# Kernel tuning notes

Measured on AMD Instinct MI355X. Metric: run time of the kernel, lower is better.

## Reference

```python
import jax, jax.numpy as jnp
import numpy as np

B, S, D = 1, 4096, 512      # batch, seq, model dim
E, K, H = 64, 2, 256        # routed experts, top-k, expert hidden (moe_inter_dim)
HS = 2048                   # shared expert hidden = n_shared_experts * inter_dim
EPS = 1e-5                  # LayerNorm eps (torch default)


def setup_inputs() -> dict:
    key = jax.random.key(0)
    ks = jax.random.split(key, 16)
    n = lambda k, shp, s=0.02: jax.random.normal(k, shp, dtype=jnp.float32) * s
    return {
        "x": jax.random.normal(ks[0], (B, S, D), dtype=jnp.float32),
        # gate Linear(dim -> E)
        "Wg": n(ks[1], (E, D)), "bg": n(ks[2], (E,)),
        # per-expert LayerNorm affine
        "gamma": 1.0 + n(ks[3], (E, D)), "beta": n(ks[4], (E, D)),
        # per-expert SwiGLU: w1, w3: D->H ; w2: H->D
        "W1": n(ks[5], (E, D, H)), "b1": n(ks[6], (E, H)),
        "W3": n(ks[7], (E, D, H)), "b3": n(ks[8], (E, H)),
        "W2": n(ks[9], (E, H, D)), "b2": n(ks[10], (E, D)),
        # shared expert (same Expert structure, hidden HS)
        "gs": 1.0 + n(ks[11], (D,)), "bs": n(ks[11], (D,)),
        "Ws1": n(ks[12], (D, HS)), "bs1": n(ks[12], (HS,)),
        "Ws3": n(ks[13], (D, HS)), "bs3": n(ks[13], (HS,)),
        "Ws2": n(ks[14], (HS, D)), "bs2": n(ks[15], (D,)),
    }


def reference(x, Wg, bg, gamma, beta, W1, b1, W3, b3, W2, b2,
              gs, bs, Ws1, bs1, Ws3, bs3, Ws2, bs2):
    shape = x.shape
    xt = x.reshape(-1, D)                      # [T, D] tokens
    T = xt.shape[0]

    # ---- Gate (eval path: sigmoid scores, no load balancing / bias / groups) ----
    scores = jax.nn.sigmoid(xt @ Wg.T + bg)    # [T, E]
    w, idx = jax.lax.top_k(scores, K)          # [T, K]
    w = w / w.sum(-1, keepdims=True)           # sigmoid path normalization; route_scale = 1
    # dense combine weights: cw[t, e] = routing weight of token t on expert e (0 if not routed)
    cw = jnp.zeros((T, E), xt.dtype).at[jnp.arange(T)[:, None], idx].add(w)

    # ---- Shared LayerNorm statistics (affine folded per-expert below) ----
    mu = xt.mean(-1, keepdims=True)
    var = ((xt - mu) ** 2).mean(-1, keepdims=True)
    nx = (xt - mu) * jax.lax.rsqrt(var + EPS)  # [T, D], unit-affine normalized

    # Fold each expert's LN affine (gamma_e, beta_e) into its w1/w3:
    # (nx*g + b) @ W = nx @ (g[:,None]*W) + b @ W
    W1p = gamma[:, :, None] * W1
    b1p = b1 + jnp.einsum('ed,edh->eh', beta, W1)
    W3p = gamma[:, :, None] * W3
    b3p = b3 + jnp.einsum('ed,edh->eh', beta, W3)

    h1 = jnp.einsum('td,edh->eth', nx, W1p) + b1p[:, None, :]   # [E, T, H]
    h3 = jnp.einsum('td,edh->eth', nx, W3p) + b3p[:, None, :]
    h = jax.nn.silu(h1) * h3                                     # SwiGLU, [E, T, H]

    # Weighted combine: y[t] = sum_e cw[t,e] * (h[e,t] @ W2[e] + b2[e])
    hw = h * cw.T[:, :, None]                                    # [E, T, H]
    y = jnp.einsum('eth,ehd->td', hw, W2) + cw @ b2              # [T, D]

    # ---- Shared expert (applied to every token) ----
    nxs = nx * gs + bs
    hs = jax.nn.silu(nxs @ Ws1 + bs1) * (nxs @ Ws3 + bs3)        # [T, HS]
    z = hs @ Ws2 + bs2

    return (y + z).reshape(shape)
```

## Files before the change

### kernel.cpp

```cpp
#include <hip/hip_runtime.h>
#include <math.h>

typedef unsigned short u16;
typedef unsigned int u32;
typedef __attribute__((ext_vector_type(8))) short bf16x8;
typedef __attribute__((ext_vector_type(4))) float f32x4;

#define TT   4096
#define DM   512
#define NE   64
#define HE   256
#define HSH  2048
#define NSH  8
#define PADBASE 16384
#define MAXTILES 384

#define WAITV(N) asm volatile("s_waitcnt vmcnt(" #N ")" ::: "memory")
#define SBAR()   __builtin_amdgcn_s_barrier()
#define SCHEDB() __builtin_amdgcn_sched_barrier(0)

__device__ __forceinline__ float sig_(float z){ return 1.f/(1.f+__expf(-z)); }

__device__ __forceinline__ u16 f2bf(float x){
  u32 u = __builtin_bit_cast(u32, x);
  u = (u + 0x7FFFu + ((u >> 16) & 1u)) >> 16;
  return (u16)u;
}

__device__ __forceinline__ f32x4 mfma16(bf16x8 a, bf16x8 b, f32x4 c){
  return __builtin_amdgcn_mfma_f32_16x16x32_bf16(a, b, c, 0, 0, 0);
}

__device__ __forceinline__ bf16x8 frd(const char* tile, int row, int csw){
  return *(const bf16x8*)(tile + row*64 + csw);
}

__device__ __forceinline__ void gl16(const void* g, void* l){
  __builtin_amdgcn_global_load_lds(
      (const __attribute__((address_space(1))) unsigned int*)g,
      (__attribute__((address_space(3))) unsigned int*)l, 16, 0, 0);
}

template<int K, int N, bool FOLD>
__device__ __forceinline__ void cvt_tile(
    const float* __restrict__ in, const float* __restrict__ scale,
    const float* __restrict__ fvec, u16* __restrict__ out,
    float* __restrict__ fout, int local, int tid, char* LT)
{
  const int nbk = K >> 6;
  const int nbn = N >> 8;
  const int pm = nbk * nbn;
  const int z = local / pm, rem = local - z*pm;
  const int kt = rem % nbk, ntile = rem / nbk;
  const int k0 = kt*64;
  const int q = tid >> 6;
  const int t = tid & 63;
  const int nb = t*4;

  const float* src = in + (size_t)z*K*N + (size_t)(k0 + q*16)*N + ntile*256 + nb;
  const float* scp = scale ? (scale + (size_t)z*K + k0 + q*16) : nullptr;
  const float* fvp = fvec  ? (fvec  + (size_t)z*K + k0 + q*16) : nullptr;

  u32 pk[4][8];
  float fs0=0.f, fs1=0.f, fs2=0.f, fs3=0.f;
  #pragma unroll
  for (int j = 0; j < 16; j++){
    float4 v = *(const float4*)(src + (size_t)j*N);
    const float sc = scp ? scp[j] : 1.0f;
    const u32 b0 = f2bf(v.x*sc), b1 = f2bf(v.y*sc);
    const u32 b2 = f2bf(v.z*sc), b3 = f2bf(v.w*sc);
    if (j & 1){
      pk[0][j>>1] |= b0 << 16; pk[1][j>>1] |= b1 << 16;
      pk[2][j>>1] |= b2 << 16; pk[3][j>>1] |= b3 << 16;
    } else {
      pk[0][j>>1] = b0; pk[1][j>>1] = b1;
      pk[2][j>>1] = b2; pk[3][j>>1] = b3;
    }
    if (FOLD){
      const float fv = fvp[j];
      fs0 += v.x*fv; fs1 += v.y*fv; fs2 += v.z*fv; fs3 += v.w*fv;
    }
  }
  #pragma unroll
  for (int i = 0; i < 4; i++){
    const int n = nb + i;
    char* rowp = LT + n*144;
    const int x = (n >> 3) & 7;
    *(uint4*)(rowp + (((2*q)  ^x))*16) = *(const uint4*)&pk[i][0];
    *(uint4*)(rowp + (((2*q+1)^x))*16) = *(const uint4*)&pk[i][4];
  }
  if (FOLD){
    float* fb = fout + (size_t)z*N + ntile*256 + nb;
    atomicAdd(fb+0, fs0); atomicAdd(fb+1, fs1);
    atomicAdd(fb+2, fs2); atomicAdd(fb+3, fs3);
  }
  __syncthreads();

  u16* obase = out + (size_t)z*K*N + (size_t)(ntile*256)*K + k0;
  #pragma unroll 2
  for (int cc = 0; cc < 8; cc++){
    const int g = cc*256 + tid;
    const int row = g >> 3, ch = g & 7;
    uint4 v = *(const uint4*)(LT + row*144 + ((ch ^ ((row>>3)&7))*16));
    *(uint4*)(obase + (size_t)row*K + ch*8) = v;
  }
}

__global__ __launch_bounds__(256) void k_pre(
    const float* __restrict__ W1, const float* __restrict__ W3,
    const float* __restrict__ W2, const float* __restrict__ Ws1,
    const float* __restrict__ Ws3, const float* __restrict__ Ws2,
    const float* __restrict__ gamma, const float* __restrict__ beta,
    const float* __restrict__ gs, const float* __restrict__ bsv,
    u16* __restrict__ W1bT, u16* __restrict__ W3bT, u16* __restrict__ W2bT,
    u16* __restrict__ Ws1bT, u16* __restrict__ Ws3bT, u16* __restrict__ Ws2bT,
    float* __restrict__ b1f, float* __restrict__ b3f,
    const float* __restrict__ x, const float* __restrict__ Wg,
    const float* __restrict__ bg,
    u16* __restrict__ nxb, int* __restrict__ top_idx, float* __restrict__ top_w)
{
  __shared__ __align__(16) char LT[256*144];
  const int bid = blockIdx.x;
  const int tid = threadIdx.x;

  if (bid < 1728){
    if      (bid < 512)  cvt_tile<DM,HE, true >(W1,  gamma,   beta,    W1bT,  b1f,        bid,      tid, LT);
    else if (bid < 1024) cvt_tile<DM,HE, true >(W3,  gamma,   beta,    W3bT,  b3f,        bid-512,  tid, LT);
    else if (bid < 1536) cvt_tile<HE,DM, false>(W2,  nullptr, nullptr, W2bT,  nullptr,    bid-1024, tid, LT);
    else if (bid < 1600) cvt_tile<DM,HSH,true >(Ws1, gs,      bsv,     Ws1bT, b1f+NE*HE,  bid-1536, tid, LT);
    else if (bid < 1664) cvt_tile<DM,HSH,true >(Ws3, gs,      bsv,     Ws3bT, b3f+NE*HE,  bid-1600, tid, LT);
    else                 cvt_tile<HSH,DM,false>(Ws2, nullptr, nullptr, Ws2bT, nullptr,    bid-1664, tid, LT);
    return;
  }

  __shared__ float xs[DM];
  __shared__ float sred[4], ssred[4];
  __shared__ float sc[NE];
  const int t = bid - 1728;

  float2 v = reinterpret_cast<const float2*>(x + (size_t)t*DM)[tid];
  xs[2*tid]   = v.x;
  xs[2*tid+1] = v.y;
  float s  = v.x + v.y;
  float ss = v.x*v.x + v.y*v.y;
  #pragma unroll
  for (int o = 32; o > 0; o >>= 1){ s += __shfl_xor(s, o); ss += __shfl_xor(ss, o); }
  const int wid = tid >> 6, lane = tid & 63;
  if (lane == 0){ sred[wid] = s; ssred[wid] = ss; }
  __syncthreads();
  const float tot = sred[0]+sred[1]+sred[2]+sred[3];
  const float tss = ssred[0]+ssred[1]+ssred[2]+ssred[3];
  const float mu  = tot * (1.f/DM);
  const float var = tss * (1.f/DM) - mu*mu;
  const float rstd = rsqrtf(var + 1e-5f);
  u32 pk = (u32)f2bf((v.x-mu)*rstd) | ((u32)f2bf((v.y-mu)*rstd) << 16);
  *(u32*)(nxb + (size_t)t*DM + 2*tid) = pk;

  const int e = tid >> 2, sub = tid & 3;
  const float4* wrow4 = reinterpret_cast<const float4*>(Wg + (size_t)e*DM);
  const float4* xs4   = reinterpret_cast<const float4*>(xs);
  float acc = 0.f;
  #pragma unroll 4
  for (int i = sub; i < DM/4; i += 4){
    const float4 w = wrow4[i]; const float4 xv = xs4[i];
    acc += xv.x*w.x + xv.y*w.y + xv.z*w.z + xv.w*w.w;
  }
  acc += __shfl_xor(acc, 1);
  acc += __shfl_xor(acc, 2);
  if (sub == 0) sc[e] = acc + bg[e];
  __syncthreads();

  if (tid < 64) {
    const float s0 = sc[tid];
    float m = s0; int mi = tid;
    #pragma unroll
    for (int o = 1; o < 64; o <<= 1){
      float om = __shfl_xor(m, o); int oi = __shfl_xor(mi, o);
      if (om > m || (om == m && oi < mi)) { m = om; mi = oi; }
    }
    float s1 = (tid == mi) ? -INFINITY : s0;
    float m2 = s1; int mi2 = tid;
    #pragma unroll
    for (int o = 1; o < 64; o <<= 1){
      float om = __shfl_xor(m2, o); int oi = __shfl_xor(mi2, o);
      if (om > m2 || (om == m2 && oi < mi2)) { m2 = om; mi2 = oi; }
    }
    if (tid == 0){
      const float w0 = sig_(m), w1 = sig_(m2);
      const float inv = 1.f/(w0+w1);
      top_idx[2*t]   = mi;
      top_idx[2*t+1] = mi2;
      top_w[2*t]     = w0*inv;
      top_w[2*t+1]   = w1*inv;
    }
  }
}

__global__ __launch_bounds__(256) void k_route(
    const int* __restrict__ top_idx, const float* __restrict__ top_w,
    int* __restrict__ bucket_tok, float* __restrict__ bucket_w,
    int* __restrict__ tiles, int* __restrict__ n_tiles)
{
  __shared__ int cnt[NE], base_[NE];
  __shared__ int nroute;
  const int tid = threadIdx.x;
  if (tid < NE) cnt[tid] = 0;
  __syncthreads();
  for (int p = tid; p < TT*2; p += 256) atomicAdd(&cnt[top_idx[p]], 1);
  __syncthreads();
  if (tid == 0){
    int run = 0, ntl = 0;
    for (int e = 0; e < NE; e++){
      base_[e] = run;
      const int c = cnt[e];
      for (int b = 0; b < c; b += 128){
        const int n = (c - b < 128) ? (c - b) : 128;
        tiles[ntl++] = (e << 17) | (((run + b) >> 7) << 8) | n;
      }
      run += ((c + 127) >> 7) << 7;
    }
    nroute = ntl;
    n_tiles[0] = ntl + NSH*(TT/128);
    n_tiles[1] = ntl;
  }
  __syncthreads();
  if (tid < NSH*(TT/128)){
    const int s = tid >> 5, t = tid & 31;
    const int b0 = PADBASE + s*TT + t*128;
    tiles[nroute + tid] = ((NE + s) << 17) | ((b0 >> 7) << 8) | 128;
  }
  if (tid < NE) cnt[tid] = 0;
  __syncthreads();
  for (int p = tid; p < TT*2; p += 256){
    const int e = top_idx[p];
    const int pos = base_[e] + atomicAdd(&cnt[e], 1);
    bucket_tok[pos] = p >> 1;
    bucket_w[pos]   = top_w[p];
  }
}

__global__ __launch_bounds__(512) void k_up(
    const u16* __restrict__ nxb,
    const u16* __restrict__ W1bT, const u16* __restrict__ W3bT,
    const u16* __restrict__ Ws1bT, const u16* __restrict__ Ws3bT,
    const float* __restrict__ b1, const float* __restrict__ b3,
    const float* __restrict__ bs1, const float* __restrict__ bs3,
    const float* __restrict__ b1f, const float* __restrict__ b3f,
    const int* __restrict__ bucket_tok, const float* __restrict__ bucket_w,
    const int* __restrict__ tiles, const int* __restrict__ n_tiles,
    u16* __restrict__ hrout, u16* __restrict__ hs)
{
  if ((int)blockIdx.x >= n_tiles[0]) return;
  const int info = tiles[blockIdx.x];
  const int e  = info >> 17;
  const int b0 = ((info >> 8) & 0x1FF) << 7;
  const int nt = info & 255;
  const bool sh = (e >= NE);
  const int y  = blockIdx.y;

  __shared__ __align__(16) char Ab[2][8192];
  __shared__ __align__(16) char B1b[2][8192];
  __shared__ __align__(16) char B3b[2][8192];
  __shared__ int   toks[128];
  __shared__ float tw[128];

  const int tid = threadIdx.x, wid = tid >> 6, lane = tid & 63;
  const int l15 = lane & 15, q = lane >> 4;

  if (tid < 128){
    int tk; float w;
    if (!sh){
      if (tid < nt){ tk = bucket_tok[b0+tid]; w = bucket_w[b0+tid]; }
      else         { tk = 0; w = 0.f; }
    } else {
      tk = ((b0 - PADBASE) & (TT-1)) + tid; w = 1.f;
    }
    toks[tid] = tk; tw[tid] = w;
  }
  __syncthreads();

  const u16* w1e = sh ? (Ws1bT + (size_t)(e-NE)*HE*DM) : (W1bT + (size_t)e*HE*DM);
  const u16* w3e = sh ? (Ws3bT + (size_t)(e-NE)*HE*DM) : (W3bT + (size_t)e*HE*DM);

  const int srow = lane >> 2;
  const int csrc = (((lane & 3) ^ ((lane >> 3) & 3))) * 8;
  const u16* asrc = nxb + (size_t)toks[wid*16 + srow]*DM + csrc;
  const u16* b1s  = w1e + (size_t)(y*128 + wid*16 + srow)*DM + csrc;
  const u16* b3s  = w3e + (size_t)(y*128 + wid*16 + srow)*DM + csrc;
  const int loff = wid*1024;

#define UP_STAGE(ph, k0) do{ \
    gl16(asrc + (k0), Ab[ph] + loff); \
    gl16(b1s  + (k0), B1b[ph] + loff); \
    gl16(b3s  + (k0), B3b[ph] + loff); \
  } while(0)

  const int wm = (wid & 1)*64, wn = (wid >> 1)*32;

  const float* ob1 = sh ? (bs1 + (size_t)(e-NE)*HE) : (b1 + (size_t)e*HE);
  const float* ob3 = sh ? (bs3 + (size_t)(e-NE)*HE) : (b3 + (size_t)e*HE);
  f32x4 acc1[4][2], acc3[4][2];
  #pragma unroll
  for (int fn = 0; fn < 2; fn++){
    const int h = y*128 + wn + fn*16 + l15;
    const float v1 = ob1[h] + b1f[(size_t)e*HE + h];
    const float v3 = ob3[h] + b3f[(size_t)e*HE + h];
    #pragma unroll
    for (int fm = 0; fm < 4; fm++){
      acc1[fm][fn] = (f32x4){v1,v1,v1,v1};
      acc3[fm][fn] = (f32x4){v3,v3,v3,v3};
    }
  }

  UP_STAGE(0, 0);
  const int csw = (q ^ ((l15 >> 1) & 3)) * 16;

  for (int ks = 0; ks < DM/32; ks++){
    const int cur = ks & 1;
    WAITV(0);
    SBAR();
    if (ks + 1 < DM/32){ UP_STAGE(cur^1, (ks+1)*32); SCHEDB(); }
    const char* A  = Ab[cur];
    const char* B1 = B1b[cur];
    const char* B3 = B3b[cur];
    __builtin_amdgcn_s_setprio(1);
    bf16x8 fa[4];
    #pragma unroll
    for (int fm = 0; fm < 4; fm++) fa[fm] = frd(A, wm + fm*16 + l15, csw);
    #pragma unroll
    for (int fn = 0; fn < 2; fn++){
      bf16x8 fb1 = frd(B1, wn + fn*16 + l15, csw);
      bf16x8 fb3 = frd(B3, wn + fn*16 + l15, csw);
      #pragma unroll
      for (int fm = 0; fm < 4; fm++){
        acc1[fm][fn] = mfma16(fa[fm], fb1, acc1[fm][fn]);
        acc3[fm][fn] = mfma16(fa[fm], fb3, acc3[fm][fn]);
      }
    }
    __builtin_amdgcn_s_setprio(0);
  }
#undef UP_STAGE

  const int tbase = sh ? ((b0 - PADBASE) & (TT-1)) : 0;
  const int scol  = sh ? (e - NE)*HE : 0;
  #pragma unroll
  for (int fm = 0; fm < 4; fm++){
    #pragma unroll
    for (int fn = 0; fn < 2; fn++){
      const int hl = y*128 + wn + fn*16 + l15;
      #pragma unroll
      for (int r = 0; r < 4; r++){
        const int m = wm + fm*16 + 4*q + r;
        float v = 0.f;
        if (m < nt){
          const float a1 = acc1[fm][fn][r];
          const float a3 = acc3[fm][fn][r];
          v = a1 * sig_(a1) * a3 * tw[m];
        }
        if (sh) hs[(size_t)(tbase+m)*HSH + scol + hl] = f2bf(v);
        else    hrout[(size_t)(b0+m)*HE + hl] = f2bf(v);
      }
    }
  }
}

__global__ __launch_bounds__(512) void k_down(
    const u16* __restrict__ hs, const u16* __restrict__ Ws2bT,
    const float* __restrict__ bs2,
    const u16* __restrict__ hrout, const u16* __restrict__ W2bT,
    const float* __restrict__ b2,
    const int* __restrict__ bucket_tok, const float* __restrict__ bucket_w,
    const int* __restrict__ tiles, const int* __restrict__ n_tiles,
    float* __restrict__ out)
{
  __shared__ __align__(16) char Ab[2][8192];
  __shared__ __align__(16) char Bb[2][16384];
  __shared__ int   toks[128];
  __shared__ float tw[128];

  const int tid = threadIdx.x, wid = tid >> 6, lane = tid & 63;
  const int l15 = lane & 15, q = lane >> 4;
  const int csw  = (q ^ ((l15 >> 1) & 3)) * 16;
  const int srow = tid >> 2;
  const int csrc = ((tid & 3) ^ ((tid >> 3) & 3)) * 8;
  const int loff = wid*1024;
  const int wm = (wid & 1)*64, wn = (wid >> 1)*64;

  const u16* asrc; const u16* bsrc0; const u16* bsrc1;
  int nsteps, nt, d0;
  bool shpath;
  int e = 0, b0 = 0, kc = 0;

  if ((int)blockIdx.x < 256){
    shpath = true;
    kc = blockIdx.x & 3;
    d0 = ((blockIdx.x >> 2) & 1) * 256;
    const int t0 = (blockIdx.x >> 3) * 128;
    nsteps = 16; nt = 128;
    asrc  = hs    + (size_t)(t0 + srow)*HSH + kc*512 + csrc;
    bsrc0 = Ws2bT + (size_t)(d0 + srow)*HSH + kc*512 + csrc;
    bsrc1 = Ws2bT + (size_t)(d0 + 128 + srow)*HSH + kc*512 + csrc;
    if (tid < 128){ toks[tid] = t0 + tid; tw[tid] = 1.f; }
  } else {
    shpath = false;
    const int rb = (int)blockIdx.x - 256;
    const int ti = rb >> 1;
    if (ti >= n_tiles[1]) return;
    const int info = tiles[ti];
    e  = info >> 17;
    b0 = ((info >> 8) & 0x1FF) << 7;
    nt = info & 255;
    d0 = (rb & 1) * 256;
    nsteps = 8;
    const u16* w2e = W2bT + (size_t)e*DM*HE;
    asrc  = hrout + (size_t)(b0 + srow)*HE + csrc;
    bsrc0 = w2e + (size_t)(d0 + srow)*HE + csrc;
    bsrc1 = w2e + (size_t)(d0 + 128 + srow)*HE + csrc;
    if (tid < 128){
      if (tid < nt){ toks[tid] = bucket_tok[b0+tid]; tw[tid] = bucket_w[b0+tid]; }
      else         { toks[tid] = 0; tw[tid] = 0.f; }
    }
  }
  const size_t lda = shpath ? HSH : HE;
  (void)lda;
  __syncthreads();

#define DN_STAGE(ph, k0) do{ \
    gl16(asrc  + (k0), Ab[ph] + loff); \
    gl16(bsrc0 + (k0), Bb[ph] + loff); \
    gl16(bsrc1 + (k0), Bb[ph] + 8192 + loff); \
  } while(0)

  f32x4 acc[4][4];
  #pragma unroll
  for (int fm = 0; fm < 4; fm++)
    #pragma unroll
    for (int fn = 0; fn < 4; fn++) acc[fm][fn] = (f32x4){0.f,0.f,0.f,0.f};

  DN_STAGE(0, 0);

  for (int ks = 0; ks < nsteps; ks++){
    const int cur = ks & 1;
    WAITV(0);
    SBAR();
    if (ks + 1 < nsteps){ DN_STAGE(cur^1, (ks+1)*32); SCHEDB(); }
    const char* A = Ab[cur];
    const char* B = Bb[cur];
    __builtin_amdgcn_s_setprio(1);
    bf16x8 fa[4];
    #pragma unroll
    for (int fm = 0; fm < 4; fm++) fa[fm] = frd(A, wm + fm*16 + l15, csw);
    #pragma unroll
    for (int fn = 0; fn < 4; fn++){
      bf16x8 fb = frd(B, wn + fn*16 + l15, csw);
      #pragma unroll
      for (int fm = 0; fm < 4; fm++)
        acc[fm][fn] = mfma16(fa[fm], fb, acc[fm][fn]);
    }
    __builtin_amdgcn_s_setprio(0);
  }
#undef DN_STAGE

  #pragma unroll
  for (int fm = 0; fm < 4; fm++){
    #pragma unroll
    for (int fn = 0; fn < 4; fn++){
      const int d = d0 + wn + fn*16 + l15;
      float badd;
      if (shpath) badd = (kc == 0) ? bs2[d] : 0.f;
      else        badd = 0.f;
      #pragma unroll
      for (int r = 0; r < 4; r++){
        const int m = wm + fm*16 + 4*q + r;
        if (m < nt){
          const float extra = shpath ? badd : tw[m]*b2[(size_t)e*DM + d];
          atomicAdd(out + (size_t)toks[m]*DM + d, acc[fm][fn][r] + extra);
        }
      }
    }
  }
}

extern "C" void kernel_launch(void* const* d_in, const int* in_sizes, int n_in,
                              void* d_out, int out_size, void* d_ws, size_t ws_size,
                              hipStream_t stream)
{
  (void)in_sizes; (void)n_in; (void)ws_size;
  const float* x     = (const float*)d_in[0];
  const float* Wg    = (const float*)d_in[1];
  const float* bg    = (const float*)d_in[2];
  const float* gamma = (const float*)d_in[3];
  const float* beta  = (const float*)d_in[4];
  const float* W1    = (const float*)d_in[5];
  const float* b1    = (const float*)d_in[6];
  const float* W3    = (const float*)d_in[7];
  const float* b3    = (const float*)d_in[8];
  const float* W2    = (const float*)d_in[9];
  const float* b2    = (const float*)d_in[10];
  const float* gs    = (const float*)d_in[11];
  const float* bs    = (const float*)d_in[12];
  const float* Ws1   = (const float*)d_in[13];
  const float* bs1   = (const float*)d_in[14];
  const float* Ws3   = (const float*)d_in[15];
  const float* bs3   = (const float*)d_in[16];
  const float* Ws2   = (const float*)d_in[17];
  const float* bs2   = (const float*)d_in[18];
  float* out = (float*)d_out;

  char* ws = (char*)d_ws;
  size_t off = 0;
  auto alloc = [&](size_t bytes) -> char* {
    char* p = ws + off;
    off += (bytes + 255) & ~(size_t)255;
    return p;
  };
  u16*   nxb        = (u16*)  alloc((size_t)TT*DM*2);
  int*   top_idx    = (int*)  alloc((size_t)TT*2*4);
  float* top_w      = (float*)alloc((size_t)TT*2*4);
  int*   bucket_tok = (int*)  alloc((size_t)PADBASE*4);
  float* bucket_w   = (float*)alloc((size_t)PADBASE*4);
  int*   tiles      = (int*)  alloc(MAXTILES*4);
  int*   n_tiles    = (int*)  alloc(64);
  u16*   hrout      = (u16*)  alloc((size_t)PADBASE*HE*2);
  u16*   hs         = (u16*)  alloc((size_t)TT*HSH*2);
  u16*   W1bT       = (u16*)  alloc((size_t)NE*HE*DM*2);
  u16*   W3bT       = (u16*)  alloc((size_t)NE*HE*DM*2);
  u16*   W2bT       = (u16*)  alloc((size_t)NE*DM*HE*2);
  u16*   Ws1bT      = (u16*)  alloc((size_t)HSH*DM*2);
  u16*   Ws3bT      = (u16*)  alloc((size_t)HSH*DM*2);
  u16*   Ws2bT      = (u16*)  alloc((size_t)DM*HSH*2);
  float* b1f        = (float*)alloc((size_t)(NE*HE + HSH)*4);
  float* b3f        = (float*)alloc((size_t)(NE*HE + HSH)*4);

  hipMemsetAsync(b1f, 0, (size_t)(NE*HE + HSH)*4, stream);
  hipMemsetAsync(b3f, 0, (size_t)(NE*HE + HSH)*4, stream);
  hipMemsetAsync(out, 0, (size_t)out_size*sizeof(float), stream);

  k_pre<<<dim3(1728 + TT), 256, 0, stream>>>(
      W1, W3, W2, Ws1, Ws3, Ws2, gamma, beta, gs, bs,
      W1bT, W3bT, W2bT, Ws1bT, Ws3bT, Ws2bT, b1f, b3f,
      x, Wg, bg, nxb, top_idx, top_w);

  k_route<<<dim3(1), 256, 0, stream>>>(top_idx, top_w, bucket_tok, bucket_w, tiles, n_tiles);

  k_up<<<dim3(MAXTILES, 2), 512, 0, stream>>>(nxb, W1bT, W3bT, Ws1bT, Ws3bT,
                                              b1, b3, bs1, bs3, b1f, b3f,
                                              bucket_tok, bucket_w, tiles, n_tiles, hrout, hs);
  k_down<<<dim3(512), 512, 0, stream>>>(hs, Ws2bT, bs2, hrout, W2bT, b2,
                                        bucket_tok, bucket_w, tiles, n_tiles, out);
}
```

Measured before the change: 205.1 us.

## Shrink k_down tiles to 128x128 with 256 threads and batch cvt_tile loads

The down-projection kernel goes from 512-thread blocks computing 128x256 output tiles to 256-thread blocks computing 128x128 tiles, which doubles the grid and halves shared memory per block. The aim is more blocks in flight and better occupancy. The cost is that each A tile is loaded twice as often across the grid, and the number of atomic adds stays the same. Separately, the weight-conversion prologue now issues eight float4 loads at a time and loads the scale and fold vectors as float4, so more memory requests are in flight together.

Result: slower. 225.1 us (+9.8%).

```diff
diff --git a/kernel.cpp b/kernel.cpp
--- a/kernel.cpp
+++ b/kernel.cpp
@@ -58,29 +58,45 @@
   const int nb = t*4;
 
   const float* src = in + (size_t)z*K*N + (size_t)(k0 + q*16)*N + ntile*256 + nb;
-  const float* scp = scale ? (scale + (size_t)z*K + k0 + q*16) : nullptr;
-  const float* fvp = fvec  ? (fvec  + (size_t)z*K + k0 + q*16) : nullptr;
+  const float* scp = FOLD ? (scale + (size_t)z*K + k0 + q*16) : nullptr;
+  const float* fvp = FOLD ? (fvec  + (size_t)z*K + k0 + q*16) : nullptr;
 
   u32 pk[4][8];
   float fs0=0.f, fs1=0.f, fs2=0.f, fs3=0.f;
-  #pragma unroll
-  for (int j = 0; j < 16; j++){
-    float4 v = *(const float4*)(src + (size_t)j*N);
-    const float sc = scp ? scp[j] : 1.0f;
-    const u32 b0 = f2bf(v.x*sc), b1 = f2bf(v.y*sc);
-    const u32 b2 = f2bf(v.z*sc), b3 = f2bf(v.w*sc);
-    if (j & 1){
-      pk[0][j>>1] |= b0 << 16; pk[1][j>>1] |= b1 << 16;
-      pk[2][j>>1] |= b2 << 16; pk[3][j>>1] |= b3 << 16;
-    } else {
-      pk[0][j>>1] = b0; pk[1][j>>1] = b1;
-      pk[2][j>>1] = b2; pk[3][j>>1] = b3;
-    }
+
+  #pragma unroll
+  for (int half = 0; half < 2; half++){
+    float4 v[8];
+    #pragma unroll
+    for (int j = 0; j < 8; j++)
+      v[j] = *(const float4*)(src + (size_t)(half*8 + j)*N);
+    float scv[8], fvv[8];
     if (FOLD){
-      const float fv = fvp[j];
-      fs0 += v.x*fv; fs1 += v.y*fv; fs2 += v.z*fv; fs3 += v.w*fv;
-    }
-  }
+      *(float4*)&scv[0] = *(const float4*)(scp + half*8);
+      *(float4*)&scv[4] = *(const float4*)(scp + half*8 + 4);
+      *(float4*)&fvv[0] = *(const float4*)(fvp + half*8);
+      *(float4*)&fvv[4] = *(const float4*)(fvp + half*8 + 4);
+    }
+    #pragma unroll
+    for (int j = 0; j < 8; j++){
+      const int jj = half*8 + j;
+      const float sc = FOLD ? scv[j] : 1.0f;
+      const u32 b0 = f2bf(v[j].x*sc), b1 = f2bf(v[j].y*sc);
+      const u32 b2 = f2bf(v[j].z*sc), b3 = f2bf(v[j].w*sc);
+      if (jj & 1){
+        pk[0][jj>>1] |= b0 << 16; pk[1][jj>>1] |= b1 << 16;
+        pk[2][jj>>1] |= b2 << 16; pk[3][jj>>1] |= b3 << 16;
+      } else {
+        pk[0][jj>>1] = b0; pk[1][jj>>1] = b1;
+        pk[2][jj>>1] = b2; pk[3][jj>>1] = b3;
+      }
+      if (FOLD){
+        const float fv = fvv[j];
+        fs0 += v[j].x*fv; fs1 += v[j].y*fv; fs2 += v[j].z*fv; fs3 += v[j].w*fv;
+      }
+    }
+  }
+
   #pragma unroll
   for (int i = 0; i < 4; i++){
     const int n = nb + i;
@@ -364,7 +380,7 @@
   }
 }
 
-__global__ __launch_bounds__(512) void k_down(
+__global__ __launch_bounds__(256) void k_down(
     const u16* __restrict__ hs, const u16* __restrict__ Ws2bT,
     const float* __restrict__ bs2,
     const u16* __restrict__ hrout, const u16* __restrict__ W2bT,
@@ -374,7 +390,7 @@
     float* __restrict__ out)
 {
   __shared__ __align__(16) char Ab[2][8192];
-  __shared__ __align__(16) char Bb[2][16384];
+  __shared__ __align__(16) char Bb[2][8192];
   __shared__ int   toks[128];
   __shared__ float tw[128];
 
@@ -386,49 +402,50 @@
   const int loff = wid*1024;
   const int wm = (wid & 1)*64, wn = (wid >> 1)*64;
 
-  const u16* asrc; const u16* bsrc0; const u16* bsrc1;
+  const u16 *asrc, *asrc2, *bsrc, *bsrc2;
   int nsteps, nt, d0;
   bool shpath;
-  int e = 0, b0 = 0, kc = 0;
-
-  if ((int)blockIdx.x < 256){
+  int e = 0, kc = 0;
+
+  if ((int)blockIdx.x < 512){
     shpath = true;
     kc = blockIdx.x & 3;
-    d0 = ((blockIdx.x >> 2) & 1) * 256;
-    const int t0 = (blockIdx.x >> 3) * 128;
+    d0 = ((blockIdx.x >> 2) & 3) * 128;
+    const int t0 = (blockIdx.x >> 4) * 128;
     nsteps = 16; nt = 128;
     asrc  = hs    + (size_t)(t0 + srow)*HSH + kc*512 + csrc;
-    bsrc0 = Ws2bT + (size_t)(d0 + srow)*HSH + kc*512 + csrc;
-    bsrc1 = Ws2bT + (size_t)(d0 + 128 + srow)*HSH + kc*512 + csrc;
+    asrc2 = asrc  + (size_t)64*HSH;
+    bsrc  = Ws2bT + (size_t)(d0 + srow)*HSH + kc*512 + csrc;
+    bsrc2 = bsrc  + (size_t)64*HSH;
     if (tid < 128){ toks[tid] = t0 + tid; tw[tid] = 1.f; }
   } else {
     shpath = false;
-    const int rb = (int)blockIdx.x - 256;
-    const int ti = rb >> 1;
+    const int rb = (int)blockIdx.x - 512;
+    const int ti = rb >> 2;
     if (ti >= n_tiles[1]) return;
     const int info = tiles[ti];
     e  = info >> 17;
-    b0 = ((info >> 8) & 0x1FF) << 7;
+    const int b0 = ((info >> 8) & 0x1FF) << 7;
     nt = info & 255;
-    d0 = (rb & 1) * 256;
+    d0 = (rb & 3) * 128;
     nsteps = 8;
     const u16* w2e = W2bT + (size_t)e*DM*HE;
     asrc  = hrout + (size_t)(b0 + srow)*HE + csrc;
-    bsrc0 = w2e + (size_t)(d0 + srow)*HE + csrc;
-    bsrc1 = w2e + (size_t)(d0 + 128 + srow)*HE + csrc;
+    asrc2 = asrc  + (size_t)64*HE;
+    bsrc  = w2e + (size_t)(d0 + srow)*HE + csrc;
+    bsrc2 = bsrc + (size_t)64*HE;
     if (tid < 128){
       if (tid < nt){ toks[tid] = bucket_tok[b0+tid]; tw[tid] = bucket_w[b0+tid]; }
       else         { toks[tid] = 0; tw[tid] = 0.f; }
     }
   }
-  const size_t lda = shpath ? HSH : HE;
-  (void)lda;
   __syncthreads();
 
 #define DN_STAGE(ph, k0) do{ \
     gl16(asrc  + (k0), Ab[ph] + loff); \
-    gl16(bsrc0 + (k0), Bb[ph] + loff); \
-    gl16(bsrc1 + (k0), Bb[ph] + 8192 + loff); \
+    gl16(asrc2 + (k0), Ab[ph] + 4096 + loff); \
+    gl16(bsrc  + (k0), Bb[ph] + loff); \
+    gl16(bsrc2 + (k0), Bb[ph] + 4096 + loff); \
   } while(0)
 
   f32x4 acc[4][4];
@@ -466,9 +483,7 @@
     #pragma unroll
     for (int fn = 0; fn < 4; fn++){
       const int d = d0 + wn + fn*16 + l15;
-      float badd;
-      if (shpath) badd = (kc == 0) ? bs2[d] : 0.f;
-      else        badd = 0.f;
+      const float badd = shpath ? ((kc == 0) ? bs2[d] : 0.f) : 0.f;
       #pragma unroll
       for (int r = 0; r < 4; r++){
         const int m = wm + fm*16 + 4*q + r;
@@ -546,6 +561,6 @@
   k_up<<<dim3(MAXTILES, 2), 512, 0, stream>>>(nxb, W1bT, W3bT, Ws1bT, Ws3bT,
                                               b1, b3, bs1, bs3, b1f, b3f,
                                               bucket_tok, bucket_w, tiles, n_tiles, hrout, hs);
-  k_down<<<dim3(512), 512, 0, stream>>>(hs, Ws2bT, bs2, hrout, W2bT, b2,
-                                        bucket_tok, bucket_w, tiles, n_tiles, out);
-}
+  k_down<<<dim3(1024), 256, 0, stream>>>(hs, Ws2bT, bs2, hrout, W2bT, b2,
+                                         bucket_tok, bucket_w, tiles, n_tiles, out);
+}
```
